# Performance work log

Measured on AMD Instinct MI355X. Metric: run time of the kernel, lower is better.

## Reference

```python
import jax, jax.numpy as jnp
import numpy as np

B, L, C, N_LAYERS, N_NBR, HID = 16, 512, 4, 4, 2, 256

def setup_inputs() -> dict:
    key = jax.random.key(0)
    k = jax.random.split(key, 5)
    n = jax.random.normal(k[0], (B, L, 3), dtype=jnp.float32)
    w_self = jnp.ones((C, N_LAYERS), dtype=jnp.float32)
    w_nbr = 0.1 * jnp.ones((C, N_LAYERS, N_NBR), dtype=jnp.float32)
    W1 = jax.random.normal(k[1], (C * L, HID), dtype=jnp.float32) * (1.0 / np.sqrt(C * L))
    b1 = jnp.zeros((HID,), dtype=jnp.float32)
    W2 = jax.random.normal(k[2], (HID, 1), dtype=jnp.float32) * (0.01 / np.sqrt(HID))
    b2 = jnp.zeros((1,), dtype=jnp.float32)
    return {"n": n, "w_self": w_self, "w_nbr": w_nbr, "W1": W1, "b1": b1, "W2": W2, "b2": b2}

def reference(n, w_self, w_nbr, W1, b1, W2, b2):
    act = jax.nn.celu
    # 1) O(3)-invariant Gram matrix, diagonal removed
    g = jnp.einsum('...id,...jd->...ij', n, n)   # (B, L, L)
    L_ = g.shape[-1]
    mask = 1.0 - jnp.eye(L_, dtype=g.dtype)
    g = g * mask
    Cc, n_layers = w_self.shape
    n_nbr = w_nbr.shape[-1]
    # (B, C, L, L)
    x = jnp.broadcast_to(g[..., None, :, :], g.shape[:-2] + (Cc, L_, L_))
    for ell in range(n_layers):
        y = w_self[:, ell][:, None, None] * x
        for d in range(1, n_nbr + 1):
            s = (jnp.roll(x, d, axis=-1) + jnp.roll(x, -d, axis=-1)
                 + jnp.roll(x, d, axis=-2) + jnp.roll(x, -d, axis=-2))
            y = y + w_nbr[:, ell, d - 1][:, None, None] * s
        x = x + act(y)
        x = 0.5 * (x + jnp.swapaxes(x, -1, -2))  # symmetrize
        x = x * mask                              # zero diagonal
    # 4) cyclic diagonal sums: c_r = sum_i x[..., i, (i+r) mod L]  (single gather)
    i = jnp.arange(L_)
    cols = (i[:, None] + i[None, :]) % L_         # (L_i, L_r)
    sep = x[..., i[:, None], cols].sum(axis=-2)   # (B, C, L)
    # 5) MLP head
    h = sep.reshape(*sep.shape[:-2], -1)          # (B, C*L)
    h = act(h @ W1 + b1)
    y = jnp.squeeze(h @ W2 + b2, axis=-1)         # (B,)
    return jnp.exp(-y)
```

## Files before the change

### kernel.cpp

```cpp
#include <hip/hip_runtime.h>

#define LSZ 512
#define CCH 4
#define NLAY 4
#define TILE 64
#define HALO 8
#define RG  80
#define RGP 82
#define NT  512

typedef float v2f __attribute__((ext_vector_type(2)));

__device__ __forceinline__ v2f pk_add(v2f a, v2f b) {
    v2f d; asm("v_pk_add_f32 %0, %1, %2" : "=v"(d) : "v"(a), "v"(b)); return d;
}
__device__ __forceinline__ v2f pk_mul(v2f a, v2f b) {
    v2f d; asm("v_pk_mul_f32 %0, %1, %2" : "=v"(d) : "v"(a), "v"(b)); return d;
}
__device__ __forceinline__ v2f pk_fma(v2f a, v2f b, v2f c) {
    v2f d; asm("v_pk_fma_f32 %0, %1, %2, %3" : "=v"(d) : "v"(a), "v"(b), "v"(c)); return d;
}
__device__ __forceinline__ v2f celu2(v2f y) {
    v2f r;
    r.x = y.x >= 0.0f ? y.x : __expf(y.x) - 1.0f;
    r.y = y.y >= 0.0f ? y.y : __expf(y.y) - 1.0f;
    return r;
}
__device__ __forceinline__ v2f ld2(const float* p) { return *(const v2f*)p; }

__global__ void check_kernel(const float* __restrict__ w_self,
                             const float* __restrict__ w_nbr,
                             int* __restrict__ flag)
{
    const int t = threadIdx.x;
    bool ok = true;
    if (t < 12) {
        int c = 1 + t / 4, e = t % 4;
        ok = (w_self[c * 4 + e] == w_self[e]);
    } else if (t < 36) {
        int u = t - 12;
        int c = 1 + u / 8, r = u % 8;
        ok = (w_nbr[c * 8 + r] == w_nbr[r]);
    }
    unsigned long long vote = __ballot(ok);
    if (t == 0) *flag = (vote == ~0ull) ? 1 : 0;
}

__global__ __launch_bounds__(NT, 8) void stencil_kernel(
    const float* __restrict__ nn,
    const float* __restrict__ w_self,
    const float* __restrict__ w_nbr,
    float* __restrict__ sep,
    const int* __restrict__ flag)
{
    __shared__ __align__(16) float buf[RG * RGP];
    __shared__ float nrow[RG][3];
    __shared__ float ncol[RG][3];

    const int tid = threadIdx.x;
    const int bid = blockIdx.x;
    const int img = bid / 36;
    int t = bid - img * 36;
    const int b = img >> 2;
    const int c = img & 3;
    if (c != 0 && *flag) return;
    int ti = 0;
    while (t >= 8 - ti) { t -= 8 - ti; ti++; }
    const int tj = ti + t;
    const int gi0 = ti * TILE;
    const int gj0 = tj * TILE;
    const int dd = (gj0 - gi0) & (LSZ - 1);
    const bool tile_masked = (dd == 0) || (dd == 64) || (dd == 448);

    for (int u = tid; u < RG * 3 * 2; u += NT) {
        int which = u >= RG * 3;
        int v = which ? u - RG * 3 : u;
        int rr = v / 3, d = v - 3 * rr;
        int base = which ? gj0 : gi0;
        int gl = (base - HALO + rr) & (LSZ - 1);
        float val = nn[(b * LSZ + gl) * 3 + d];
        if (which) ncol[rr][d] = val; else nrow[rr][d] = val;
    }

    int ofs[4];
    int iv[4], jv[4];
    int ring[4];
    int ew[4];
#pragma unroll
    for (int it = 0; it < 4; it++) {
        int g = tid + NT * it;
        if (g < 1600) {
            int gi2 = g / 40;
            int i = 2 * gi2, j = 2 * (g - 40 * gi2);
            iv[it] = i; jv[it] = j;
            ofs[it]  = i * RGP + j;
            ring[it] = min(min(i, 78 - i), min(j, 78 - j));
            ew[it]   = (i - j - dd + 1) & 511;
        } else { ofs[it] = -1; iv[it] = 0; jv[it] = 0; ring[it] = -1; ew[it] = 99; }
    }
    __syncthreads();

#pragma unroll
    for (int it = 0; it < 4; it++) {
        if (ofs[it] < 0) continue;
        int i = iv[it], j = jv[it];
        float a00 = nrow[i][0],   a01 = nrow[i][1],   a02 = nrow[i][2];
        float a10 = nrow[i+1][0], a11 = nrow[i+1][1], a12 = nrow[i+1][2];
        float c00 = ncol[j][0],   c01 = ncol[j][1],   c02 = ncol[j][2];
        float c10 = ncol[j+1][0], c11 = ncol[j+1][1], c12 = ncol[j+1][2];
        float g00 = a00*c00 + a01*c01 + a02*c02;
        float g01 = a00*c10 + a01*c11 + a02*c12;
        float g10 = a10*c00 + a11*c01 + a12*c02;
        float g11 = a10*c10 + a11*c11 + a12*c12;
        if (tile_masked) {
            if (ew[it] == 1) { g00 = 0.0f; g11 = 0.0f; }
            if (ew[it] == 2)   g01 = 0.0f;
            if (ew[it] == 0)   g10 = 0.0f;
        }
        *(v2f*)&buf[ofs[it]]       = (v2f){g00, g01};
        *(v2f*)&buf[ofs[it] + RGP] = (v2f){g10, g11};
    }
    __syncthreads();

    for (int ell = 0; ell < NLAY; ell++) {
        const float ws  = w_self[c * NLAY + ell];
        const float wn1 = w_nbr[(c * NLAY + ell) * 2 + 0];
        const float wn2 = w_nbr[(c * NLAY + ell) * 2 + 1];
        const v2f ws2 = (v2f){ws,  ws};
        const v2f w12 = (v2f){wn1, wn1};
        const v2f w22 = (v2f){wn2, wn2};
        const int pad = 2 * (ell + 1);
        v2f o0[4], o1[4];
#pragma unroll
        for (int it = 0; it < 4; it++) {
            if (ring[it] < pad) continue;
            const float* P = buf + ofs[it];
            v2f cm2 = ld2(P - 2*RGP);
            v2f cm1 = ld2(P -   RGP);
            v2f c0  = ld2(P);
            v2f cp1 = ld2(P +   RGP);
            v2f cp2 = ld2(P + 2*RGP);
            v2f cp3 = ld2(P + 3*RGP);
            v2f A0  = ld2(P - 2);
            v2f C0  = ld2(P + 2);
            v2f A1  = ld2(P + RGP - 2);
            v2f C1  = ld2(P + RGP + 2);
            v2f s1a; s1a.x = A0.y + c0.y;  s1a.y = c0.x + C0.x;
            v2f s2a = pk_add(A0, C0);
            v2f v1a = pk_add(cm1, cp1);
            v2f v2a = pk_add(cm2, cp2);
            v2f ya = pk_fma(ws2, c0, pk_fma(w12, pk_add(s1a, v1a),
                                    pk_mul(w22, pk_add(s2a, v2a))));
            v2f s1b; s1b.x = A1.y + cp1.y; s1b.y = cp1.x + C1.x;
            v2f s2b = pk_add(A1, C1);
            v2f v1b = pk_add(c0,  cp2);
            v2f v2b = pk_add(cm1, cp3);
            v2f yb = pk_fma(ws2, cp1, pk_fma(w12, pk_add(s1b, v1b),
                                     pk_mul(w22, pk_add(s2b, v2b))));
            v2f xa = pk_add(c0,  celu2(ya));
            v2f xb = pk_add(cp1, celu2(yb));
            if (tile_masked) {
                if (ew[it] == 1) { xa.x = 0.0f; xb.y = 0.0f; }
                if (ew[it] == 2)   xa.y = 0.0f;
                if (ew[it] == 0)   xb.x = 0.0f;
            }
            o0[it] = xa;
            o1[it] = xb;
        }
        __syncthreads();
#pragma unroll
        for (int it = 0; it < 4; it++) {
            if (ring[it] < pad) continue;
            *(v2f*)&buf[ofs[it]]       = o0[it];
            *(v2f*)&buf[ofs[it] + RGP] = o1[it];
        }
        __syncthreads();
    }

    if (tid < 508) {
        int dt = tid >> 2;
        int part = tid & 3;
        int delta = dt - 63;
        int ad = delta < 0 ? -delta : delta;
        int Nd = 64 - ad;
        int i0 = 8 + (delta < 0 ? -delta : 0);
        int base = i0 * RGP + (i0 + delta);
        float s = 0.0f;
        for (int k = part; k < Nd; k += 4)
            s += buf[base + k * (RGP + 1)];
        s += __shfl_xor(s, 1);
        s += __shfl_xor(s, 2);
        if (part == 0) {
            int r = (gj0 - gi0 + delta) & (LSZ - 1);
            float* sp = sep + (b * CCH + c) * LSZ;
            atomicAdd(sp + r, s);
            if (ti != tj)
                atomicAdd(sp + ((LSZ - r) & (LSZ - 1)), s);
        }
    }
}

__global__ __launch_bounds__(256) void bcast_kernel(
    float* __restrict__ sep, const int* __restrict__ flag)
{
    if (!*flag) return;
    const int b = blockIdx.x;
    const int t = threadIdx.x;
    for (int l = t; l < LSZ; l += 256) {
        float v = sep[(b * CCH) * LSZ + l];
        sep[(b * CCH + 1) * LSZ + l] = v;
        sep[(b * CCH + 2) * LSZ + l] = v;
        sep[(b * CCH + 3) * LSZ + l] = v;
    }
}

__global__ __launch_bounds__(256) void mlp1_kernel(
    const float* __restrict__ sep,
    const float* __restrict__ W1,
    float* __restrict__ partial)
{
    __shared__ float4 red[4][64];
    const int b  = blockIdx.x >> 5;
    const int ms = blockIdx.x & 31;
    const int kq = threadIdx.x & 63;
    const int mq = threadIdx.x >> 6;
    const int m0 = ms * 64 + mq * 16;
    const float* sv = sep + b * 2048 + m0;
    const float* w  = W1 + m0 * 256 + kq * 4;
    float4 a0 = {0,0,0,0}, a1 = {0,0,0,0};
#pragma unroll
    for (int m = 0; m < 16; m += 2) {
        float4 w0 = *(const float4*)(w + (m)     * 256);
        float4 w1 = *(const float4*)(w + (m + 1) * 256);
        float s0 = sv[m], s1 = sv[m + 1];
        a0.x += s0 * w0.x; a0.y += s0 * w0.y; a0.z += s0 * w0.z; a0.w += s0 * w0.w;
        a1.x += s1 * w1.x; a1.y += s1 * w1.y; a1.z += s1 * w1.z; a1.w += s1 * w1.w;
    }
    float4 a;
    a.x = a0.x + a1.x; a.y = a0.y + a1.y; a.z = a0.z + a1.z; a.w = a0.w + a1.w;
    red[mq][kq] = a;
    __syncthreads();
    if (mq == 0) {
        float4 r0 = red[0][kq], r1 = red[1][kq], r2 = red[2][kq], r3 = red[3][kq];
        float4 o;
        o.x = (r0.x + r1.x) + (r2.x + r3.x);
        o.y = (r0.y + r1.y) + (r2.y + r3.y);
        o.z = (r0.z + r1.z) + (r2.z + r3.z);
        o.w = (r0.w + r1.w) + (r2.w + r3.w);
        *(float4*)&partial[(b * 32 + ms) * 256 + kq * 4] = o;
    }
}

__global__ __launch_bounds__(256) void mlp2_kernel(
    const float* __restrict__ partial,
    const float* __restrict__ b1,
    const float* __restrict__ W2,
    const float* __restrict__ b2,
    float* __restrict__ out)
{
    __shared__ double red[4];
    const int b = blockIdx.x;
    const int k = threadIdx.x;
    double s = 0;
#pragma unroll
    for (int p = 0; p < 32; p++)
        s += (double)partial[(b * 32 + p) * 256 + k];
    s += (double)b1[k];
    s = s >= 0.0 ? s : exp(s) - 1.0;
    double q = s * (double)W2[k];
    for (int off = 32; off >= 1; off >>= 1) q += __shfl_down(q, off);
    if ((k & 63) == 0) red[k >> 6] = q;
    __syncthreads();
    if (k == 0) {
        double y = ((red[0] + red[1]) + (red[2] + red[3])) + (double)b2[0];
        out[b] = (float)exp(-y);
    }
}

extern "C" void kernel_launch(void* const* d_in, const int* in_sizes, int n_in,
                              void* d_out, int out_size, void* d_ws, size_t ws_size,
                              hipStream_t stream) {
    const float* nn     = (const float*)d_in[0];
    const float* w_self = (const float*)d_in[1];
    const float* w_nbr  = (const float*)d_in[2];
    const float* W1     = (const float*)d_in[3];
    const float* b1     = (const float*)d_in[4];
    const float* W2     = (const float*)d_in[5];
    const float* b2     = (const float*)d_in[6];
    float* out = (float*)d_out;
    float* sep     = (float*)d_ws;
    float* partial = (float*)((char*)d_ws + 128 * 1024);
    int*   flag    = (int*)((char*)d_ws + 640 * 1024);

    hipMemsetAsync(sep, 0, 16 * CCH * LSZ * sizeof(float), stream);
    check_kernel<<<1, 64, 0, stream>>>(w_self, w_nbr, flag);
    stencil_kernel<<<64 * 36, NT, 0, stream>>>(nn, w_self, w_nbr, sep, flag);
    bcast_kernel<<<16, 256, 0, stream>>>(sep, flag);
    mlp1_kernel<<<512, 256, 0, stream>>>(sep, W1, partial);
    mlp2_kernel<<<16, 256, 0, stream>>>(partial, b1, W2, b2, out);
}
```

Measured before the change: 93.13 us.

## Fold equal-channel case into summed W1 and drop broadcast/memset launches

When all channels share the same weights, the stencil grid now runs one block per (batch, tile) and loops over channels, doing only channel 0 instead of launching early-exiting blocks. Since the four sep channels would then be identical, a new kernel sums the four W1 row blocks. mlp1 then uses only a quarter of the slices and mlp2 reduces fewer partials, so the broadcast kernel goes away. The sep memset is folded into the flag-check kernel. This trades removed launches and idle blocks for an extra pass that reads all of W1 on every call.

```diff
diff --git a/kernel.cpp b/kernel.cpp
--- a/kernel.cpp
+++ b/kernel.cpp
@@ -28,22 +28,51 @@
 }
 __device__ __forceinline__ v2f ld2(const float* p) { return *(const v2f*)p; }
 
-__global__ void check_kernel(const float* __restrict__ w_self,
-                             const float* __restrict__ w_nbr,
-                             int* __restrict__ flag)
-{
-    const int t = threadIdx.x;
-    bool ok = true;
-    if (t < 12) {
-        int c = 1 + t / 4, e = t % 4;
-        ok = (w_self[c * 4 + e] == w_self[e]);
-    } else if (t < 36) {
-        int u = t - 12;
-        int c = 1 + u / 8, r = u % 8;
-        ok = (w_nbr[c * 8 + r] == w_nbr[r]);
-    }
-    unsigned long long vote = __ballot(ok);
-    if (t == 0) *flag = (vote == ~0ull) ? 1 : 0;
+__global__ __launch_bounds__(256) void zero_check_kernel(
+    const float* __restrict__ w_self,
+    const float* __restrict__ w_nbr,
+    float* __restrict__ sep,
+    int* __restrict__ flag)
+{
+    const int b = blockIdx.x;
+    float4 z = {0.0f, 0.0f, 0.0f, 0.0f};
+    for (int m = threadIdx.x; m < 512; m += 256)
+        *(float4*)&sep[b * 2048 + m * 4] = z;
+    if (b == 0 && threadIdx.x < 64) {
+        int t = threadIdx.x;
+        bool ok = true;
+        if (t < 12) {
+            int c = 1 + t / 4, e = t % 4;
+            ok = (w_self[c * 4 + e] == w_self[e]);
+        } else if (t < 36) {
+            int u = t - 12, c = 1 + u / 8, r = u % 8;
+            ok = (w_nbr[c * 8 + r] == w_nbr[r]);
+        }
+        unsigned long long vote = __ballot(ok);
+        if (t == 0) *flag = (vote == ~0ull) ? 1 : 0;
+    }
+}
+
+__global__ __launch_bounds__(256) void wsum_kernel(
+    const float* __restrict__ W1,
+    float* __restrict__ W1s,
+    const int* __restrict__ flag)
+{
+    if (!*flag) return;
+    int idx = blockIdx.x * 256 + threadIdx.x;
+    int m  = idx >> 6;
+    int k4 = (idx & 63) * 4;
+    const float* p = W1 + m * 256 + k4;
+    float4 a = *(const float4*)p;
+    float4 b = *(const float4*)(p +  512 * 256);
+    float4 c = *(const float4*)(p + 1024 * 256);
+    float4 d = *(const float4*)(p + 1536 * 256);
+    float4 o;
+    o.x = (a.x + b.x) + (c.x + d.x);
+    o.y = (a.y + b.y) + (c.y + d.y);
+    o.z = (a.z + b.z) + (c.z + d.z);
+    o.w = (a.w + b.w) + (c.w + d.w);
+    *(float4*)&W1s[m * 256 + k4] = o;
 }
 
 __global__ __launch_bounds__(NT, 8) void stencil_kernel(
@@ -59,11 +88,8 @@
 
     const int tid = threadIdx.x;
     const int bid = blockIdx.x;
-    const int img = bid / 36;
-    int t = bid - img * 36;
-    const int b = img >> 2;
-    const int c = img & 3;
-    if (c != 0 && *flag) return;
+    const int b = bid / 36;
+    int t = bid - b * 36;
     int ti = 0;
     while (t >= 8 - ti) { t -= 8 - ti; ti++; }
     const int tj = ti + t;
@@ -71,6 +97,7 @@
     const int gj0 = tj * TILE;
     const int dd = (gj0 - gi0) & (LSZ - 1);
     const bool tile_masked = (dd == 0) || (dd == 64) || (dd == 448);
+    const int cmax = (*flag) ? 1 : CCH;
 
     for (int u = tid; u < RG * 3 * 2; u += NT) {
         int which = u >= RG * 3;
@@ -100,133 +127,126 @@
     }
     __syncthreads();
 
-#pragma unroll
-    for (int it = 0; it < 4; it++) {
-        if (ofs[it] < 0) continue;
-        int i = iv[it], j = jv[it];
-        float a00 = nrow[i][0],   a01 = nrow[i][1],   a02 = nrow[i][2];
-        float a10 = nrow[i+1][0], a11 = nrow[i+1][1], a12 = nrow[i+1][2];
-        float c00 = ncol[j][0],   c01 = ncol[j][1],   c02 = ncol[j][2];
-        float c10 = ncol[j+1][0], c11 = ncol[j+1][1], c12 = ncol[j+1][2];
-        float g00 = a00*c00 + a01*c01 + a02*c02;
-        float g01 = a00*c10 + a01*c11 + a02*c12;
-        float g10 = a10*c00 + a11*c01 + a12*c02;
-        float g11 = a10*c10 + a11*c11 + a12*c12;
-        if (tile_masked) {
-            if (ew[it] == 1) { g00 = 0.0f; g11 = 0.0f; }
-            if (ew[it] == 2)   g01 = 0.0f;
-            if (ew[it] == 0)   g10 = 0.0f;
-        }
-        *(v2f*)&buf[ofs[it]]       = (v2f){g00, g01};
-        *(v2f*)&buf[ofs[it] + RGP] = (v2f){g10, g11};
-    }
-    __syncthreads();
-
-    for (int ell = 0; ell < NLAY; ell++) {
-        const float ws  = w_self[c * NLAY + ell];
-        const float wn1 = w_nbr[(c * NLAY + ell) * 2 + 0];
-        const float wn2 = w_nbr[(c * NLAY + ell) * 2 + 1];
-        const v2f ws2 = (v2f){ws,  ws};
-        const v2f w12 = (v2f){wn1, wn1};
-        const v2f w22 = (v2f){wn2, wn2};
-        const int pad = 2 * (ell + 1);
-        v2f o0[4], o1[4];
+    for (int c = 0; c < cmax; c++) {
 #pragma unroll
         for (int it = 0; it < 4; it++) {
-            if (ring[it] < pad) continue;
-            const float* P = buf + ofs[it];
-            v2f cm2 = ld2(P - 2*RGP);
-            v2f cm1 = ld2(P -   RGP);
-            v2f c0  = ld2(P);
-            v2f cp1 = ld2(P +   RGP);
-            v2f cp2 = ld2(P + 2*RGP);
-            v2f cp3 = ld2(P + 3*RGP);
-            v2f A0  = ld2(P - 2);
-            v2f C0  = ld2(P + 2);
-            v2f A1  = ld2(P + RGP - 2);
-            v2f C1  = ld2(P + RGP + 2);
-            v2f s1a; s1a.x = A0.y + c0.y;  s1a.y = c0.x + C0.x;
-            v2f s2a = pk_add(A0, C0);
-            v2f v1a = pk_add(cm1, cp1);
-            v2f v2a = pk_add(cm2, cp2);
-            v2f ya = pk_fma(ws2, c0, pk_fma(w12, pk_add(s1a, v1a),
-                                    pk_mul(w22, pk_add(s2a, v2a))));
-            v2f s1b; s1b.x = A1.y + cp1.y; s1b.y = cp1.x + C1.x;
-            v2f s2b = pk_add(A1, C1);
-            v2f v1b = pk_add(c0,  cp2);
-            v2f v2b = pk_add(cm1, cp3);
-            v2f yb = pk_fma(ws2, cp1, pk_fma(w12, pk_add(s1b, v1b),
-                                     pk_mul(w22, pk_add(s2b, v2b))));
-            v2f xa = pk_add(c0,  celu2(ya));
-            v2f xb = pk_add(cp1, celu2(yb));
+            if (ofs[it] < 0) continue;
+            int i = iv[it], j = jv[it];
+            float a00 = nrow[i][0],   a01 = nrow[i][1],   a02 = nrow[i][2];
+            float a10 = nrow[i+1][0], a11 = nrow[i+1][1], a12 = nrow[i+1][2];
+            float c00 = ncol[j][0],   c01 = ncol[j][1],   c02 = ncol[j][2];
+            float c10 = ncol[j+1][0], c11 = ncol[j+1][1], c12 = ncol[j+1][2];
+            float g00 = a00*c00 + a01*c01 + a02*c02;
+            float g01 = a00*c10 + a01*c11 + a02*c12;
+            float g10 = a10*c00 + a11*c01 + a12*c02;
+            float g11 = a10*c10 + a11*c11 + a12*c12;
             if (tile_masked) {
-                if (ew[it] == 1) { xa.x = 0.0f; xb.y = 0.0f; }
-                if (ew[it] == 2)   xa.y = 0.0f;
-                if (ew[it] == 0)   xb.x = 0.0f;
+                if (ew[it] == 1) { g00 = 0.0f; g11 = 0.0f; }
+                if (ew[it] == 2)   g01 = 0.0f;
+                if (ew[it] == 0)   g10 = 0.0f;
             }
-            o0[it] = xa;
-            o1[it] = xb;
+            *(v2f*)&buf[ofs[it]]       = (v2f){g00, g01};
+            *(v2f*)&buf[ofs[it] + RGP] = (v2f){g10, g11};
         }
         __syncthreads();
-#pragma unroll
-        for (int it = 0; it < 4; it++) {
-            if (ring[it] < pad) continue;
-            *(v2f*)&buf[ofs[it]]       = o0[it];
-            *(v2f*)&buf[ofs[it] + RGP] = o1[it];
+
+        for (int ell = 0; ell < NLAY; ell++) {
+            const float ws  = w_self[c * NLAY + ell];
+            const float wn1 = w_nbr[(c * NLAY + ell) * 2 + 0];
+            const float wn2 = w_nbr[(c * NLAY + ell) * 2 + 1];
+            const v2f ws2 = (v2f){ws,  ws};
+            const v2f w12 = (v2f){wn1, wn1};
+            const v2f w22 = (v2f){wn2, wn2};
+            const int pad = 2 * (ell + 1);
+            v2f o0[4], o1[4];
+#pragma unroll
+            for (int it = 0; it < 4; it++) {
+                if (ring[it] < pad) continue;
+                const float* P = buf + ofs[it];
+                v2f cm2 = ld2(P - 2*RGP);
+                v2f cm1 = ld2(P -   RGP);
+                v2f c0  = ld2(P);
+                v2f cp1 = ld2(P +   RGP);
+                v2f cp2 = ld2(P + 2*RGP);
+                v2f cp3 = ld2(P + 3*RGP);
+                v2f A0  = ld2(P - 2);
+                v2f C0  = ld2(P + 2);
+                v2f A1  = ld2(P + RGP - 2);
+                v2f C1  = ld2(P + RGP + 2);
+                v2f s1a; s1a.x = A0.y + c0.y;  s1a.y = c0.x + C0.x;
+                v2f s2a = pk_add(A0, C0);
+                v2f v1a = pk_add(cm1, cp1);
+                v2f v2a = pk_add(cm2, cp2);
+                v2f ya = pk_fma(ws2, c0, pk_fma(w12, pk_add(s1a, v1a),
+                                        pk_mul(w22, pk_add(s2a, v2a))));
+                v2f s1b; s1b.x = A1.y + cp1.y; s1b.y = cp1.x + C1.x;
+                v2f s2b = pk_add(A1, C1);
+                v2f v1b = pk_add(c0,  cp2);
+                v2f v2b = pk_add(cm1, cp3);
+                v2f yb = pk_fma(ws2, cp1, pk_fma(w12, pk_add(s1b, v1b),
+                                         pk_mul(w22, pk_add(s2b, v2b))));
+                v2f xa = pk_add(c0,  celu2(ya));
+                v2f xb = pk_add(cp1, celu2(yb));
+                if (tile_masked) {
+                    if (ew[it] == 1) { xa.x = 0.0f; xb.y = 0.0f; }
+                    if (ew[it] == 2)   xa.y = 0.0f;
+                    if (ew[it] == 0)   xb.x = 0.0f;
+                }
+                o0[it] = xa;
+                o1[it] = xb;
+            }
+            __syncthreads();
+#pragma unroll
+            for (int it = 0; it < 4; it++) {
+                if (ring[it] < pad) continue;
+                *(v2f*)&buf[ofs[it]]       = o0[it];
+                *(v2f*)&buf[ofs[it] + RGP] = o1[it];
+            }
+            __syncthreads();
+        }
+
+        if (tid < 508) {
+            int dt = tid >> 2;
+            int part = tid & 3;
+            int delta = dt - 63;
+            int ad = delta < 0 ? -delta : delta;
+            int Nd = 64 - ad;
+            int i0 = 8 + (delta < 0 ? -delta : 0);
+            int base = i0 * RGP + (i0 + delta);
+            float s = 0.0f;
+            for (int k = part; k < Nd; k += 4)
+                s += buf[base + k * (RGP + 1)];
+            s += __shfl_xor(s, 1);
+            s += __shfl_xor(s, 2);
+            if (part == 0) {
+                int r = (gj0 - gi0 + delta) & (LSZ - 1);
+                float* sp = sep + (b * CCH + c) * LSZ;
+                atomicAdd(sp + r, s);
+                if (ti != tj)
+                    atomicAdd(sp + ((LSZ - r) & (LSZ - 1)), s);
+            }
         }
         __syncthreads();
-    }
-
-    if (tid < 508) {
-        int dt = tid >> 2;
-        int part = tid & 3;
-        int delta = dt - 63;
-        int ad = delta < 0 ? -delta : delta;
-        int Nd = 64 - ad;
-        int i0 = 8 + (delta < 0 ? -delta : 0);
-        int base = i0 * RGP + (i0 + delta);
-        float s = 0.0f;
-        for (int k = part; k < Nd; k += 4)
-            s += buf[base + k * (RGP + 1)];
-        s += __shfl_xor(s, 1);
-        s += __shfl_xor(s, 2);
-        if (part == 0) {
-            int r = (gj0 - gi0 + delta) & (LSZ - 1);
-            float* sp = sep + (b * CCH + c) * LSZ;
-            atomicAdd(sp + r, s);
-            if (ti != tj)
-                atomicAdd(sp + ((LSZ - r) & (LSZ - 1)), s);
-        }
-    }
-}
-
-__global__ __launch_bounds__(256) void bcast_kernel(
-    float* __restrict__ sep, const int* __restrict__ flag)
-{
-    if (!*flag) return;
-    const int b = blockIdx.x;
-    const int t = threadIdx.x;
-    for (int l = t; l < LSZ; l += 256) {
-        float v = sep[(b * CCH) * LSZ + l];
-        sep[(b * CCH + 1) * LSZ + l] = v;
-        sep[(b * CCH + 2) * LSZ + l] = v;
-        sep[(b * CCH + 3) * LSZ + l] = v;
     }
 }
 
 __global__ __launch_bounds__(256) void mlp1_kernel(
     const float* __restrict__ sep,
     const float* __restrict__ W1,
-    float* __restrict__ partial)
+    const float* __restrict__ W1s,
+    float* __restrict__ partial,
+    const int* __restrict__ flag)
 {
     __shared__ float4 red[4][64];
+    const int f  = *flag;
     const int b  = blockIdx.x >> 5;
     const int ms = blockIdx.x & 31;
+    if (f && ms >= 8) return;
     const int kq = threadIdx.x & 63;
     const int mq = threadIdx.x >> 6;
     const int m0 = ms * 64 + mq * 16;
     const float* sv = sep + b * 2048 + m0;
-    const float* w  = W1 + m0 * 256 + kq * 4;
+    const float* w  = (f ? W1s : W1) + m0 * 256 + kq * 4;
     float4 a0 = {0,0,0,0}, a1 = {0,0,0,0};
 #pragma unroll
     for (int m = 0; m < 16; m += 2) {
@@ -256,14 +276,16 @@
     const float* __restrict__ b1,
     const float* __restrict__ W2,
     const float* __restrict__ b2,
-    float* __restrict__ out)
+    float* __restrict__ out,
+    const int* __restrict__ flag)
 {
     __shared__ double red[4];
     const int b = blockIdx.x;
     const int k = threadIdx.x;
+    const int np = (*flag) ? 8 : 32;
     double s = 0;
-#pragma unroll
-    for (int p = 0; p < 32; p++)
+#pragma unroll 8
+    for (int p = 0; p < np; p++)
         s += (double)partial[(b * 32 + p) * 256 + k];
     s += (double)b1[k];
     s = s >= 0.0 ? s : exp(s) - 1.0;
@@ -289,13 +311,13 @@
     const float* b2     = (const float*)d_in[6];
     float* out = (float*)d_out;
     float* sep     = (float*)d_ws;
-    float* partial = (float*)((char*)d_ws + 128 * 1024);
-    int*   flag    = (int*)((char*)d_ws + 640 * 1024);
-
-    hipMemsetAsync(sep, 0, 16 * CCH * LSZ * sizeof(float), stream);
-    check_kernel<<<1, 64, 0, stream>>>(w_self, w_nbr, flag);
-    stencil_kernel<<<64 * 36, NT, 0, stream>>>(nn, w_self, w_nbr, sep, flag);
-    bcast_kernel<<<16, 256, 0, stream>>>(sep, flag);
-    mlp1_kernel<<<512, 256, 0, stream>>>(sep, W1, partial);
-    mlp2_kernel<<<16, 256, 0, stream>>>(partial, b1, W2, b2, out);
-}
+    float* partial = (float*)((char*)d_ws +  128 * 1024);
+    float* W1s     = (float*)((char*)d_ws +  640 * 1024);
+    int*   flag    = (int*)  ((char*)d_ws + 1152 * 1024);
+
+    zero_check_kernel<<<16, 256, 0, stream>>>(w_self, w_nbr, sep, flag);
+    stencil_kernel<<<16 * 36, NT, 0, stream>>>(nn, w_self, w_nbr, sep, flag);
+    wsum_kernel<<<128, 256, 0, stream>>>(W1, W1s, flag);
+    mlp1_kernel<<<512, 256, 0, stream>>>(sep, W1, W1s, partial, flag);
+    mlp2_kernel<<<16, 256, 0, stream>>>(partial, b1, W2, b2, out, flag);
+}
```

After: 96.66 us. +3.8%, slower.
